# Performance work log

Hardware: AMD Instinct MI355X
Metric: run time of the kernel (lower is better)

Reference implementation:

```python
import jax, jax.numpy as jnp
import numpy as np

SIZE = 512
WIDTH_TILES = 1
N_STROKES = 16
STROKE_WIDTH = 0.04
N_SAMPLES = 32


def setup_inputs() -> dict:
    key = jax.random.key(0)
    # matches torch.rand(n_free,4,2)*0.6+0.2 init
    control_points = jax.random.uniform(key, (N_STROKES, 4, 2), dtype=jnp.float32) * 0.6 + 0.2
    ys = jnp.linspace(0.0, 1.0, SIZE)
    xs = jnp.linspace(0.0, 1.0, SIZE * WIDTH_TILES)
    grid_y, grid_x = jnp.meshgrid(ys, xs, indexing='ij')
    pixel_grid = jnp.stack([grid_x, grid_y], axis=-1).reshape(-1, 2).astype(jnp.float32)  # [HW,2]
    return {"control_points": control_points, "pixel_grid": pixel_grid}


def _bezier3_samples(curves):
    # curves: [S,4,2] -> [S,N_SAMPLES,2]
    ts = jnp.linspace(0.0, 1.0, N_SAMPLES, dtype=curves.dtype)
    t = ts[None, :, None]
    mt = 1.0 - t
    p0, p1, p2, p3 = (curves[:, k:k + 1, :] for k in range(4))
    return mt ** 3 * p0 + 3 * mt ** 2 * t * p1 + 3 * mt * t ** 2 * p2 + t ** 3 * p3


def reference(control_points, pixel_grid):
    pts = jnp.clip(control_points, 0.0, 1.0)  # all_strokes(), symmetric=False, no groups
    pts_flat = _bezier3_samples(pts).reshape(-1, 2)  # [P,2], P = S*N_SAMPLES
    sharpness = float(N_SAMPLES) * 8.0
    # pairwise pixel-to-sample distances: [HW,P]
    diff = pixel_grid[:, None, :] - pts_flat[None, :, :]
    dist = jnp.sqrt(jnp.sum(diff * diff, axis=-1))
    # softmin via logsumexp
    min_dist = -jax.scipy.special.logsumexp(-sharpness * dist, axis=-1) / sharpness  # [HW]
    coverage = jax.nn.sigmoid((STROKE_WIDTH - min_dist) * (8.0 / STROKE_WIDTH))
    return (1.0 - coverage).reshape(SIZE, SIZE * WIDTH_TILES)[None]  # (1,H,W)
```

## Files before the change

### kernel.cpp

```cpp
#include <hip/hip_runtime.h>


#define SIZE    512
#define NPAIRS  256
#define NGRP    64
#define MARGIN  0.05f
#define LOG2E   1.4426950408889634f
#define C2      (256.0f * LOG2E)
#define FART2   0.009025f

typedef float v2f __attribute__((ext_vector_type(2)));
typedef float v4f __attribute__((ext_vector_type(4)));

__device__ __forceinline__ float sqrt_raw(float x) { return __builtin_amdgcn_sqrtf(x); }
__device__ __forceinline__ float exp2_raw(float x) { return __builtin_amdgcn_exp2f(x); }
__device__ __forceinline__ float log2_raw(float x) { return __builtin_amdgcn_logf(x); }
__device__ __forceinline__ float rcp_raw(float x)  { return __builtin_amdgcn_rcpf(x); }
__device__ __forceinline__ float clamp01(float x)  { return fminf(fmaxf(x, 0.0f), 1.0f); }

__global__ __launch_bounds__(256) void bezier_glyph_kernel(
    const float* __restrict__ cp,
    const float* __restrict__ grid,
    float* __restrict__ out)
{
    __shared__ v4f sxy[NPAIRS];
    __shared__ v2f sp2[NPAIRS];
    __shared__ v4f sbox[NGRP];
    __shared__ v4f srep[NGRP];

    const int tid = threadIdx.x;

    {
        float px[2], py[2], pq[2];
#pragma unroll
        for (int k = 0; k < 2; ++k) {
            const int i = 2 * tid + k;
            const int stroke = i >> 5, samp = i & 31;
            const float t  = (float)samp * (1.0f / 31.0f);
            const float mt = 1.0f - t;
            const float b0 = mt * mt * mt;
            const float b1 = 3.0f * mt * mt * t;
            const float b2 = 3.0f * mt * t * t;
            const float b3 = t * t * t;
            const float* p = cp + stroke * 8;
            px[k] = b0 * clamp01(p[0]) + b1 * clamp01(p[2]) + b2 * clamp01(p[4]) + b3 * clamp01(p[6]);
            py[k] = b0 * clamp01(p[1]) + b1 * clamp01(p[3]) + b2 * clamp01(p[5]) + b3 * clamp01(p[7]);
            pq[k] = px[k] * px[k] + py[k] * py[k];
        }
        sxy[tid] = (v4f){px[0], px[1], py[0], py[1]};
        sp2[tid] = (v2f){pq[0], pq[1]};
    }
    __syncthreads();

    if (tid < NGRP) {
        float lox = 1e30f, loy = 1e30f, hix = -1e30f, hiy = -1e30f;
#pragma unroll
        for (int k = 0; k < 4; ++k) {
            const v4f a = sxy[(tid << 2) + k];
            lox = fminf(lox, fminf(a.x, a.y));
            hix = fmaxf(hix, fmaxf(a.x, a.y));
            loy = fminf(loy, fminf(a.z, a.w));
            hiy = fmaxf(hiy, fmaxf(a.z, a.w));
        }
        sbox[tid] = (v4f){lox, loy, hix, hiy};
        const v4f a1 = sxy[(tid << 2) + 1];
        const v4f a3 = sxy[(tid << 2) + 3];
        srep[tid] = (v4f){a1.x, a1.z, a3.x, a3.z};
    }
    __syncthreads();

    const int lane = tid & 63;
    const int wv   = tid >> 6;
    const int px0 = (blockIdx.x << 4) + ((wv & 1) << 3);
    const int py0 = (blockIdx.y << 4) + ((wv & 2) << 2);
    const int x = px0 + (lane & 7);
    const int y = py0 + (lane >> 3);
    const float2 g = reinterpret_cast<const float2*>(grid)[y * SIZE + x];

    const float inv511 = 1.0f / 511.0f;
    const float rx0 = (float)px0 * inv511, rx1 = (float)(px0 + 7) * inv511;
    const float ry0 = (float)py0 * inv511, ry1 = (float)(py0 + 7) * inv511;
    const float cxr = 0.5f * (rx0 + rx1);
    const float cyr = 0.5f * (ry0 + ry1);
    const float hd  = 0.009686f;

    const v4f b = sbox[lane];
    const float bdx = fmaxf(fmaxf(b.x - rx1, rx0 - b.z), 0.0f);
    const float bdy = fmaxf(fmaxf(b.y - ry1, ry0 - b.w), 0.0f);
    const float db2 = bdx * bdx + bdy * bdy;

    float mdb = db2;
#pragma unroll
    for (int s = 1; s < 64; s <<= 1) mdb = fminf(mdb, __shfl_xor(mdb, s));
    if (mdb > FART2) {
        out[y * SIZE + x] = 1.0f;
        return;
    }

    const v4f r = srep[lane];
    const float d1x = cxr - r.x, d1y = cyr - r.y;
    const float d2x = cxr - r.z, d2y = cyr - r.w;
    float dc = sqrt_raw(fminf(d1x * d1x + d1y * d1y, d2x * d2x + d2y * d2y));
#pragma unroll
    for (int s = 1; s < 64; s <<= 1) dc = fminf(dc, __shfl_xor(dc, s));
    const float ub  = dc + hd;
    const float tau = ub + MARGIN;
    const unsigned long long mask = __ballot(db2 < tau * tau);

    const float n2gx = -2.0f * g.x;
    const float n2gy = -2.0f * g.y;
    const float g2   = g.x * g.x + g.y * g.y;
    const v2f   g2v  = {g2, g2};
    const float bias = C2 * ub;

    float s0 = 0.0f, s1 = 0.0f;
    {
        unsigned long long mm = mask;
        while (mm) {
            const int gi = __ffsll(mm) - 1;
            mm &= mm - 1;
            const int base = gi << 2;
#pragma unroll
            for (int k = 0; k < 4; ++k) {
                const v4f a = sxy[base + k];
                const v2f q = sp2[base + k];
                const v2f u = (v2f){a.x, a.y} * n2gx + ((v2f){a.z, a.w} * n2gy + q);
                const v2f d2v = u + g2v;
                const float da = sqrt_raw(fmaxf(d2v.x, 0.0f));
                const float db = sqrt_raw(fmaxf(d2v.y, 0.0f));
                s0 += exp2_raw(__builtin_fmaf(-C2, da, bias));
                s1 += exp2_raw(__builtin_fmaf(-C2, db, bias));
            }
        }
    }
    const float s = s0 + s1;

    const float min_dist = ub - log2_raw(s) * (1.0f / C2);
    const float z  = (0.04f - min_dist) * 200.0f;
    const float ez = exp2_raw(z * LOG2E);
    out[y * SIZE + x] = rcp_raw(1.0f + ez);
}

extern "C" void kernel_launch(void* const* d_in, const int* in_sizes, int n_in,
                              void* d_out, int out_size, void* d_ws, size_t ws_size,
                              hipStream_t stream) {
    const float* cp   = (const float*)d_in[0];
    const float* grid = (const float*)d_in[1];
    float* out = (float*)d_out;

    dim3 grid_dim(SIZE / 16, SIZE / 16);
    bezier_glyph_kernel<<<grid_dim, 256, 0, stream>>>(cp, grid, out);
}
```

Before: 63.62 us.

## Refine culling groups to 4 samples and scatter wave tiles across blocks

```diff
diff --git a/kernel.cpp b/kernel.cpp
--- a/kernel.cpp
+++ b/kernel.cpp
@@ -3,7 +3,7 @@
 
 #define SIZE    512
 #define NPAIRS  256
-#define NGRP    64
+#define NGRP    128
 #define MARGIN  0.05f
 #define LOG2E   1.4426950408889634f
 #define C2      (256.0f * LOG2E)
@@ -53,29 +53,24 @@
     __syncthreads();
 
     if (tid < NGRP) {
-        float lox = 1e30f, loy = 1e30f, hix = -1e30f, hiy = -1e30f;
-#pragma unroll
-        for (int k = 0; k < 4; ++k) {
-            const v4f a = sxy[(tid << 2) + k];
-            lox = fminf(lox, fminf(a.x, a.y));
-            hix = fmaxf(hix, fmaxf(a.x, a.y));
-            loy = fminf(loy, fminf(a.z, a.w));
-            hiy = fmaxf(hiy, fmaxf(a.z, a.w));
-        }
+        const v4f a0 = sxy[2 * tid];
+        const v4f a1 = sxy[2 * tid + 1];
+        const float lox = fminf(fminf(a0.x, a0.y), fminf(a1.x, a1.y));
+        const float hix = fmaxf(fmaxf(a0.x, a0.y), fmaxf(a1.x, a1.y));
+        const float loy = fminf(fminf(a0.z, a0.w), fminf(a1.z, a1.w));
+        const float hiy = fmaxf(fmaxf(a0.z, a0.w), fmaxf(a1.z, a1.w));
         sbox[tid] = (v4f){lox, loy, hix, hiy};
-        const v4f a1 = sxy[(tid << 2) + 1];
-        const v4f a3 = sxy[(tid << 2) + 3];
-        srep[tid] = (v4f){a1.x, a1.z, a3.x, a3.z};
+        srep[tid] = (v4f){a0.y, a0.w, a1.x, a1.z};
     }
     __syncthreads();
 
     const int lane = tid & 63;
     const int wv   = tid >> 6;
-    const int px0 = (blockIdx.x << 4) + ((wv & 1) << 3);
-    const int py0 = (blockIdx.y << 4) + ((wv & 2) << 2);
+    const int rect = ((wv << 10 | blockIdx.x) * 2897) & 4095;
+    const int px0 = (rect & 63) << 3;
+    const int py0 = (rect >> 6) << 3;
     const int x = px0 + (lane & 7);
     const int y = py0 + (lane >> 3);
-    const float2 g = reinterpret_cast<const float2*>(grid)[y * SIZE + x];
 
     const float inv511 = 1.0f / 511.0f;
     const float rx0 = (float)px0 * inv511, rx1 = (float)(px0 + 7) * inv511;
@@ -84,12 +79,16 @@
     const float cyr = 0.5f * (ry0 + ry1);
     const float hd  = 0.009686f;
 
-    const v4f b = sbox[lane];
-    const float bdx = fmaxf(fmaxf(b.x - rx1, rx0 - b.z), 0.0f);
-    const float bdy = fmaxf(fmaxf(b.y - ry1, ry0 - b.w), 0.0f);
-    const float db2 = bdx * bdx + bdy * bdy;
+    const v4f b0 = sbox[lane];
+    const v4f b1 = sbox[lane + 64];
+    const float bdx0 = fmaxf(fmaxf(b0.x - rx1, rx0 - b0.z), 0.0f);
+    const float bdy0 = fmaxf(fmaxf(b0.y - ry1, ry0 - b0.w), 0.0f);
+    const float db2_0 = bdx0 * bdx0 + bdy0 * bdy0;
+    const float bdx1 = fmaxf(fmaxf(b1.x - rx1, rx0 - b1.z), 0.0f);
+    const float bdy1 = fmaxf(fmaxf(b1.y - ry1, ry0 - b1.w), 0.0f);
+    const float db2_1 = bdx1 * bdx1 + bdy1 * bdy1;
 
-    float mdb = db2;
+    float mdb = fminf(db2_0, db2_1);
 #pragma unroll
     for (int s = 1; s < 64; s <<= 1) mdb = fminf(mdb, __shfl_xor(mdb, s));
     if (mdb > FART2) {
@@ -97,16 +96,27 @@
         return;
     }
 
-    const v4f r = srep[lane];
-    const float d1x = cxr - r.x, d1y = cyr - r.y;
-    const float d2x = cxr - r.z, d2y = cyr - r.w;
-    float dc = sqrt_raw(fminf(d1x * d1x + d1y * d1y, d2x * d2x + d2y * d2y));
+    const v4f r0 = srep[lane];
+    const v4f r1 = srep[lane + 64];
+    float dr;
+    {
+        const float e0x = cxr - r0.x, e0y = cyr - r0.y;
+        const float e1x = cxr - r0.z, e1y = cyr - r0.w;
+        const float e2x = cxr - r1.x, e2y = cyr - r1.y;
+        const float e3x = cxr - r1.z, e3y = cyr - r1.w;
+        dr = fminf(fminf(e0x * e0x + e0y * e0y, e1x * e1x + e1y * e1y),
+                   fminf(e2x * e2x + e2y * e2y, e3x * e3x + e3y * e3y));
+    }
+    float dc = sqrt_raw(dr);
 #pragma unroll
     for (int s = 1; s < 64; s <<= 1) dc = fminf(dc, __shfl_xor(dc, s));
     const float ub  = dc + hd;
     const float tau = ub + MARGIN;
-    const unsigned long long mask = __ballot(db2 < tau * tau);
+    const float tau2 = tau * tau;
+    const unsigned long long mask_lo = __ballot(db2_0 < tau2);
+    const unsigned long long mask_hi = __ballot(db2_1 < tau2);
 
+    const float2 g = reinterpret_cast<const float2*>(grid)[y * SIZE + x];
     const float n2gx = -2.0f * g.x;
     const float n2gy = -2.0f * g.y;
     const float g2   = g.x * g.x + g.y * g.y;
@@ -114,14 +124,16 @@
     const float bias = C2 * ub;
 
     float s0 = 0.0f, s1 = 0.0f;
-    {
-        unsigned long long mm = mask;
+#pragma unroll
+    for (int h = 0; h < 2; ++h) {
+        unsigned long long mm = h ? mask_hi : mask_lo;
+        const int goff = h << 6;
         while (mm) {
             const int gi = __ffsll(mm) - 1;
             mm &= mm - 1;
-            const int base = gi << 2;
+            const int base = (goff + gi) << 1;
 #pragma unroll
-            for (int k = 0; k < 4; ++k) {
+            for (int k = 0; k < 2; ++k) {
                 const v4f a = sxy[base + k];
                 const v2f q = sp2[base + k];
                 const v2f u = (v2f){a.x, a.y} * n2gx + ((v2f){a.z, a.w} * n2gy + q);
@@ -148,6 +160,5 @@
     const float* grid = (const float*)d_in[1];
     float* out = (float*)d_out;
 
-    dim3 grid_dim(SIZE / 16, SIZE / 16);
-    bezier_glyph_kernel<<<grid_dim, 256, 0, stream>>>(cp, grid, out);
+    bezier_glyph_kernel<<<1024, 256, 0, stream>>>(cp, grid, out);
 }
```

After: 62.44 us. About the same (-1.9%).
